# Kernel optimization log

Hardware: AMD Instinct MI355X
Metric: run time of the kernel (lower is better)

## Reference

```python
import jax, jax.numpy as jnp
import numpy as np

D_MODEL, N_HEADS, D_FF, THETA, EPS = 1024, 16, 4096, 10000.0, 1e-5
D_K = D_MODEL // N_HEADS


def setup_inputs() -> dict:
    key = jax.random.key(0)
    ks = jax.random.split(key, 10)

    def lin(k, out_f, in_f):
        sigma = np.sqrt(2.0 / (in_f + out_f))
        return (jax.random.truncated_normal(k, -3.0, 3.0, (out_f, in_f), jnp.float32) * sigma)

    return {
        'in_features': jax.random.normal(ks[0], (2, 2048, D_MODEL), jnp.float32),
        'Wq': lin(ks[1], D_MODEL, D_MODEL),
        'Wk': lin(ks[2], D_MODEL, D_MODEL),
        'Wv': lin(ks[3], D_MODEL, D_MODEL),
        'Wo': lin(ks[4], D_MODEL, D_MODEL),
        'ln1_w': jnp.ones((D_MODEL,), jnp.float32),
        'ln2_w': jnp.ones((D_MODEL,), jnp.float32),
        'w1': lin(ks[5], D_FF, D_MODEL),
        'w2': lin(ks[6], D_MODEL, D_FF),
        'w3': lin(ks[7], D_FF, D_MODEL),
    }


def _rmsnorm(x, w):
    xf = x.astype(jnp.float32)
    out = xf * jax.lax.rsqrt(jnp.mean(xf * xf, axis=-1, keepdims=True) + EPS) * w
    return out.astype(x.dtype)


def _rope(x, positions):
    # x: [b, h, s, d_k]; rotate pairs (2k, 2k+1) by angle pos / theta^(2k/d_k)
    k = jnp.arange(D_K // 2, dtype=jnp.float32)
    inv_freq = jnp.power(THETA, -2.0 * k / D_K)              # [d_k/2]
    ang = positions[:, None].astype(jnp.float32) * inv_freq  # [s, d_k/2]
    cos, sin = jnp.cos(ang), jnp.sin(ang)
    x_e, x_o = x[..., 0::2], x[..., 1::2]
    out_e = x_e * cos - x_o * sin
    out_o = x_e * sin + x_o * cos
    return jnp.stack([out_e, out_o], axis=-1).reshape(x.shape)


def _attention(x, Wq, Wk, Wv, Wo):
    b, s, _ = x.shape
    pos = jnp.arange(s)

    def heads(W):
        h = jnp.einsum('bsd,ed->bse', x, W)
        return h.reshape(b, s, N_HEADS, D_K).transpose(0, 2, 1, 3)  # [b,h,s,dk]

    q = _rope(heads(Wq), pos)
    k = _rope(heads(Wk), pos)
    v = heads(Wv)
    scores = jnp.einsum('bhqd,bhkd->bhqk', q, k) / jnp.sqrt(jnp.float32(D_K))
    causal = jnp.tril(jnp.ones((s, s), bool))
    scores = jnp.where(causal, scores, -jnp.inf)
    probs = jax.nn.softmax(scores, axis=-1)
    ctx = jnp.einsum('bhqk,bhkd->bhqd', probs, v)
    ctx = ctx.transpose(0, 2, 1, 3).reshape(b, s, D_MODEL)
    return jnp.einsum('bsv,dv->bsd', ctx, Wo)


def _swiglu(x, w1, w2, w3):
    a = jnp.einsum('bsd,fd->bsf', x, w1)
    g = jnp.einsum('bsd,fd->bsf', x, w3)
    return jnp.einsum('bsf,df->bsd', (a * jax.nn.sigmoid(a)) * g, w2)


def reference(in_features, Wq, Wk, Wv, Wo, ln1_w, ln2_w, w1, w2, w3):
    x = in_features + _attention(_rmsnorm(in_features, ln1_w), Wq, Wk, Wv, Wo)
    return x + _swiglu(_rmsnorm(x, ln2_w), w1, w2, w3)
```

## Files before the change

kernel.cpp:

```cpp
#include <hip/hip_runtime.h>
#include <hip/hip_bf16.h>
#include <math.h>


#define S_SEQ 2048
#define DM    1024
#define NH    16
#define DK    64
#define DFF   4096
#define T_TOK 4096

typedef short s16x8 __attribute__((ext_vector_type(8)));
typedef float f32x4 __attribute__((ext_vector_type(4)));

__device__ __forceinline__ unsigned short f32_to_bf16_rn(float f) {
  unsigned int u = __float_as_uint(f);
  unsigned int r = (u + 0x7FFFu + ((u >> 16) & 1u)) >> 16;
  return (unsigned short)r;
}
__device__ __forceinline__ float bf16_to_f32(unsigned short h) {
  return __uint_as_float(((unsigned int)h) << 16);
}

__device__ __forceinline__ void gload_lds16(const void* g, void* l) {
  __builtin_amdgcn_global_load_lds(
      (const __attribute__((address_space(1))) void*)g,
      (__attribute__((address_space(3))) void*)l, 16, 0, 0);
}

__global__ __launch_bounds__(256) void rmsnorm_planes(
    const float* __restrict__ x, const float* __restrict__ w,
    unsigned short* __restrict__ oh, unsigned short* __restrict__ ol)
{
  const int row = blockIdx.x;
  const int tid = threadIdx.x;
  const float4 v = ((const float4*)(x + (size_t)row * DM))[tid];
  float ss = v.x * v.x + v.y * v.y + v.z * v.z + v.w * v.w;
#pragma unroll
  for (int off = 32; off > 0; off >>= 1) ss += __shfl_xor(ss, off);
  __shared__ float red[4];
  if ((tid & 63) == 0) red[tid >> 6] = ss;
  __syncthreads();
  const float total = red[0] + red[1] + red[2] + red[3];
  const float scale = rsqrtf(total * (1.0f / DM) + 1e-5f);
  const float4 wv = ((const float4*)w)[tid];
  const float o0 = v.x * scale * wv.x, o1 = v.y * scale * wv.y;
  const float o2 = v.z * scale * wv.z, o3 = v.w * scale * wv.w;
  ushort4 h, l;
  h.x = f32_to_bf16_rn(o0); l.x = f32_to_bf16_rn(o0 - bf16_to_f32(h.x));
  h.y = f32_to_bf16_rn(o1); l.y = f32_to_bf16_rn(o1 - bf16_to_f32(h.y));
  h.z = f32_to_bf16_rn(o2); l.z = f32_to_bf16_rn(o2 - bf16_to_f32(h.z));
  h.w = f32_to_bf16_rn(o3); l.w = f32_to_bf16_rn(o3 - bf16_to_f32(h.w));
  ((ushort4*)(oh + (size_t)row * DM))[tid] = h;
  ((ushort4*)(ol + (size_t)row * DM))[tid] = l;
}

__global__ __launch_bounds__(256) void split_planes(
    const float* __restrict__ x, unsigned short* __restrict__ oh,
    unsigned short* __restrict__ ol, int n4)
{
  const int i = blockIdx.x * 256 + threadIdx.x;
  if (i >= n4) return;
  const float4 v = ((const float4*)x)[i];
  ushort4 h, l;
  h.x = f32_to_bf16_rn(v.x); l.x = f32_to_bf16_rn(v.x - bf16_to_f32(h.x));
  h.y = f32_to_bf16_rn(v.y); l.y = f32_to_bf16_rn(v.y - bf16_to_f32(h.y));
  h.z = f32_to_bf16_rn(v.z); l.z = f32_to_bf16_rn(v.z - bf16_to_f32(h.z));
  h.w = f32_to_bf16_rn(v.w); l.w = f32_to_bf16_rn(v.w - bf16_to_f32(h.w));
  ((ushort4*)oh)[i] = h;
  ((ushort4*)ol)[i] = l;
}

template <int MODE>
__global__ __launch_bounds__(256, 2) void gemm_sb(
    const unsigned short* __restrict__ Ah, const unsigned short* __restrict__ Al,
    const unsigned short* __restrict__ Bh, const unsigned short* __restrict__ Bl,
    const float* __restrict__ auxF,
    const unsigned short* __restrict__ auxH, const unsigned short* __restrict__ auxL,
    float* __restrict__ Cf, unsigned short* __restrict__ CH, unsigned short* __restrict__ CL,
    int N, int Kiter, int LDA, int LDB)
{
  __shared__ __align__(128) char lds[32768];
  constexpr int AHo = 0, ALo = 8192, BHo = 16384, BLo = 24576;

  const int nbn = N >> 7;
  int bid = blockIdx.x;
  const int cpx = gridDim.x >> 3;
  bid = (bid & 7) * cpx + (bid >> 3);
  const int bmi = bid / nbn;
  const int bm = bmi << 7;
  const int bn = (bid - bmi * nbn) << 7;

  const int tid  = threadIdx.x;
  const int lane = tid & 63;
  const int wave = tid >> 6;
  const int wr = (wave >> 1) << 6;
  const int wc = (wave & 1) << 6;
  const int lrow = lane & 15;
  const int lk   = lane >> 4;

  const int idx0 = tid, idx1 = tid + 256;
  const int r0 = idx0 >> 2, r1 = idx1 >> 2;
  const int c0 = idx0 & 3,  c1 = idx1 & 3;
  const size_t a0 = (size_t)(bm + r0) * LDA + c0 * 8;
  const size_t a1 = (size_t)(bm + r1) * LDA + c1 * 8;
  const size_t b0 = (size_t)(bn + r0) * LDB + c0 * 8;
  const size_t b1 = (size_t)(bn + r1) * LDB + c1 * 8;
  char* d0 = lds + idx0 * 16;
  char* d1 = lds + idx1 * 16;

  const int fro = lrow * 64 + (lk << 4);
  const char* pA = lds + AHo + wr * 64 + fro;
  const char* pB = lds + BHo + wc * 64 + fro;

  f32x4 acc[4][4] = {};

  for (int k0 = 0; k0 < Kiter; k0 += 32) {
    gload_lds16(Ah + a0 + k0, d0 + AHo);
    gload_lds16(Ah + a1 + k0, d1 + AHo);
    gload_lds16(Al + a0 + k0, d0 + ALo);
    gload_lds16(Al + a1 + k0, d1 + ALo);
    gload_lds16(Bh + b0 + k0, d0 + BHo);
    gload_lds16(Bh + b1 + k0, d1 + BHo);
    gload_lds16(Bl + b0 + k0, d0 + BLo);
    gload_lds16(Bl + b1 + k0, d1 + BLo);
    __syncthreads();

    s16x8 aH[4], aL[4], bH[4], bL[4];
#pragma unroll
    for (int f = 0; f < 4; ++f) {
      aH[f] = *(const s16x8*)(pA + f * 1024);
      aL[f] = *(const s16x8*)(pA + f * 1024 + (ALo - AHo));
      bH[f] = *(const s16x8*)(pB + f * 1024);
      bL[f] = *(const s16x8*)(pB + f * 1024 + (BLo - BHo));
    }
#pragma unroll
    for (int mi = 0; mi < 4; ++mi)
#pragma unroll
      for (int ni = 0; ni < 4; ++ni) {
        acc[mi][ni] = __builtin_amdgcn_mfma_f32_16x16x32_bf16(aH[mi], bH[ni], acc[mi][ni], 0, 0, 0);
        acc[mi][ni] = __builtin_amdgcn_mfma_f32_16x16x32_bf16(aH[mi], bL[ni], acc[mi][ni], 0, 0, 0);
        acc[mi][ni] = __builtin_amdgcn_mfma_f32_16x16x32_bf16(aL[mi], bH[ni], acc[mi][ni], 0, 0, 0);
      }
    __syncthreads();
  }

#pragma unroll
  for (int mi = 0; mi < 4; ++mi) {
#pragma unroll
    for (int r = 0; r < 4; ++r) {
      const int row = bm + wr + mi * 16 + lk * 4 + r;
      const size_t rowo = (size_t)row * N;
#pragma unroll
      for (int ni = 0; ni < 4; ++ni) {
        const int col = bn + wc + ni * 16 + lrow;
        float v = acc[mi][ni][r];
        if constexpr (MODE == 1) v += auxF[rowo + col];
        if constexpr (MODE == 2) v = v / (1.0f + expf(-v));
        if constexpr (MODE == 3)
          v *= bf16_to_f32(auxH[rowo + col]) + bf16_to_f32(auxL[rowo + col]);
        if constexpr (MODE >= 2) {
          const unsigned short hb = f32_to_bf16_rn(v);
          CH[rowo + col] = hb;
          CL[rowo + col] = f32_to_bf16_rn(v - bf16_to_f32(hb));
        } else {
          Cf[rowo + col] = v;
        }
      }
    }
  }
}

__global__ __launch_bounds__(256) void rope_table(float* __restrict__ tab)
{
  const int idx = blockIdx.x * 256 + threadIdx.x;
  const int pos = idx >> 5;
  const int i = idx & 31;
  const float ivf = (float)pow(10000.0, -(double)i / 32.0);
  const float angf = (float)((double)pos * (double)ivf);
  double sn, cs;
  sincos((double)angf, &sn, &cs);
  tab[idx * 2]     = (float)cs;
  tab[idx * 2 + 1] = (float)sn;
}

__global__ __launch_bounds__(256) void rope_apply_planes(
    unsigned short* __restrict__ QH, unsigned short* __restrict__ QL,
    unsigned short* __restrict__ KH, unsigned short* __restrict__ KL,
    const float* __restrict__ tab)
{
  const int t = blockIdx.x;
  const int pos = t & (S_SEQ - 1);
  const size_t rb = (size_t)t * DM;
#pragma unroll
  for (int it = 0; it < 2; ++it) {
    const int p = threadIdx.x + it * 256;
    const int i = p & 31;
    const int off = ((p >> 5) << 6) + (i << 1);
    const float2 cst = ((const float2*)tab)[pos * 32 + i];
    const float c = cst.x, s = cst.y;
#pragma unroll
    for (int qk = 0; qk < 2; ++qk) {
      unsigned short* H = qk ? KH : QH;
      unsigned short* L = qk ? KL : QL;
      const unsigned int vh = *(unsigned int*)(H + rb + off);
      const unsigned int vl = *(unsigned int*)(L + rb + off);
      const float e = bf16_to_f32((unsigned short)(vh & 0xffff)) +
                      bf16_to_f32((unsigned short)(vl & 0xffff));
      const float o = bf16_to_f32((unsigned short)(vh >> 16)) +
                      bf16_to_f32((unsigned short)(vl >> 16));
      const float ne = e * c - o * s;
      const float no = e * s + o * c;
      const unsigned short h0 = f32_to_bf16_rn(ne), h1 = f32_to_bf16_rn(no);
      const unsigned short l0 = f32_to_bf16_rn(ne - bf16_to_f32(h0));
      const unsigned short l1 = f32_to_bf16_rn(no - bf16_to_f32(h1));
      *(unsigned int*)(H + rb + off) = (unsigned)h0 | ((unsigned)h1 << 16);
      *(unsigned int*)(L + rb + off) = (unsigned)l0 | ((unsigned)l1 << 16);
    }
  }
}

__global__ __launch_bounds__(256) void vt_split(
    const float* __restrict__ Vf, unsigned short* __restrict__ VtH,
    unsigned short* __restrict__ VtL)
{
  __shared__ float T[64][65];
  const int b = blockIdx.z, h = blockIdx.y, s0 = blockIdx.x * 64;
  const int tid = threadIdx.x;
#pragma unroll
  for (int p = 0; p < 4; ++p) {
    const int idx = p * 256 + tid;
    const int s = idx >> 4;
    const int d4 = (idx & 15) << 2;
    const float4 v = *(const float4*)(Vf + (size_t)(b * S_SEQ + s0 + s) * DM + h * 64 + d4);
    T[s][d4] = v.x; T[s][d4 + 1] = v.y; T[s][d4 + 2] = v.z; T[s][d4 + 3] = v.w;
  }
  __syncthreads();
  const int d = tid >> 2;
  const int sc = (tid & 3) << 4;
  unsigned int hw[8], lw[8];
#pragma unroll
  for (int j = 0; j < 8; ++j) {
    const float v0 = T[sc + 2 * j][d], v1 = T[sc + 2 * j + 1][d];
    const unsigned short h0 = f32_to_bf16_rn(v0), h1 = f32_to_bf16_rn(v1);
    const unsigned short l0 = f32_to_bf16_rn(v0 - bf16_to_f32(h0));
    const unsigned short l1 = f32_to_bf16_rn(v1 - bf16_to_f32(h1));
    hw[j] = (unsigned)h0 | ((unsigned)h1 << 16);
    lw[j] = (unsigned)l0 | ((unsigned)l1 << 16);
  }
  const size_t base = ((size_t)((b * NH + h) * 64 + d)) * S_SEQ + s0 + sc;
#pragma unroll
  for (int j = 0; j < 8; ++j) {
    *(unsigned int*)(VtH + base + 2 * j) = hw[j];
    *(unsigned int*)(VtL + base + 2 * j) = lw[j];
  }
}

__global__ __launch_bounds__(256, 3) void attn_mfma(
    const unsigned short* __restrict__ QH, const unsigned short* __restrict__ QL,
    const unsigned short* __restrict__ KH, const unsigned short* __restrict__ KL,
    const unsigned short* __restrict__ VtH, const unsigned short* __restrict__ VtL,
    unsigned short* __restrict__ ctxH, unsigned short* __restrict__ ctxL)
{
  __shared__ __align__(128) char lds[51200];
  const int h = blockIdx.y, b = blockIdx.z;
  const int qt = 31 - blockIdx.x;
  const int q0 = qt << 6;
  const int tid = threadIdx.x;
  const int lane = tid & 63;
  const int w = tid >> 6;
  const int lg = lane >> 4;
  const int lr = lane & 15;

  const size_t qtok = (size_t)(b * S_SEQ + q0 + w * 16 + lr);
  s16x8 qh[2], ql[2];
#pragma unroll
  for (int kc = 0; kc < 2; ++kc) {
    const size_t off = qtok * DM + h * 64 + kc * 32 + lg * 8;
    qh[kc] = *(const s16x8*)(QH + off);
    ql[kc] = *(const s16x8*)(QL + off);
  }

  f32x4 acc[4] = {};
  float mrow[4], lsum[4];
#pragma unroll
  for (int r = 0; r < 4; ++r) { mrow[r] = -1e30f; lsum[r] = 0.f; }

  unsigned short* PH = (unsigned short*)(lds + 32768 + w * 4608);
  unsigned short* PL = PH + 1152;
  const int wmax = q0 + w * 16 + 15;
  const int ntiles = qt + 1;

  for (int t = 0; t < ntiles; ++t) {
    const int kt = t << 6;
#pragma unroll
    for (int pp = 0; pp < 8; ++pp) {
      const int idx = pp * 256 + tid;
      const int plane = idx >> 9;
      const int ci = idx & 511;
      const int row = ci >> 3, pc = ci & 7;
      const int lc = pc ^ (row & 7);
      const unsigned short* src;
      if (plane == 0)      src = KH + (size_t)(b * S_SEQ + kt + row) * DM + h * 64 + lc * 8;
      else if (plane == 1) src = KL + (size_t)(b * S_SEQ + kt + row) * DM + h * 64 + lc * 8;
      else if (plane == 2) src = VtH + ((size_t)((b * NH + h) * 64 + row)) * S_SEQ + kt + lc * 8;
      else                 src = VtL + ((size_t)((b * NH + h) * 64 + row)) * S_SEQ + kt + lc * 8;
      gload_lds16(src, lds + plane * 8192 + ci * 16);
    }
    __syncthreads();

    if (kt <= wmax) {
      f32x4 s[4] = {};
      __builtin_amdgcn_s_setprio(1);
#pragma unroll
      for (int nf = 0; nf < 4; ++nf) {
        const int key = nf * 16 + lr;
#pragma unroll
        for (int kc = 0; kc < 2; ++kc) {
          const int pcx = (kc * 4 + lg) ^ (key & 7);
          const char* base = lds + key * 128 + pcx * 16;
          const s16x8 kh = *(const s16x8*)(base);
          const s16x8 kl = *(const s16x8*)(base + 8192);
          s[nf] = __builtin_amdgcn_mfma_f32_16x16x32_bf16(qh[kc], kh, s[nf], 0, 0, 0);
          s[nf] = __builtin_amdgcn_mfma_f32_16x16x32_bf16(qh[kc], kl, s[nf], 0, 0, 0);
          s[nf] = __builtin_amdgcn_mfma_f32_16x16x32_bf16(ql[kc], kh, s[nf], 0, 0, 0);
        }
      }
      __builtin_amdgcn_s_setprio(0);
      const int myrow = q0 + w * 16 + 4 * lg;
#pragma unroll
      for (int nf = 0; nf < 4; ++nf) {
        const int key = kt + nf * 16 + lr;
#pragma unroll
        for (int r = 0; r < 4; ++r) {
          const float sv = s[nf][r] * 0.125f;
          s[nf][r] = (key <= myrow + r) ? sv : -__builtin_inff();
        }
      }
#pragma unroll
      for (int r = 0; r < 4; ++r) {
        float mx = fmaxf(fmaxf(s[0][r], s[1][r]), fmaxf(s[2][r], s[3][r]));
        mx = fmaxf(mx, __shfl_xor(mx, 1));
        mx = fmaxf(mx, __shfl_xor(mx, 2));
        mx = fmaxf(mx, __shfl_xor(mx, 4));
        mx = fmaxf(mx, __shfl_xor(mx, 8));
        const float mn = fmaxf(mrow[r], mx);
        const float corr = __expf(mrow[r] - mn);
        mrow[r] = mn;
        float ps = 0.f;
#pragma unroll
        for (int nf = 0; nf < 4; ++nf) {
          const float pv = __expf(s[nf][r] - mn);
          s[nf][r] = pv;
          ps += pv;
        }
        ps += __shfl_xor(ps, 1); ps += __shfl_xor(ps, 2);
        ps += __shfl_xor(ps, 4); ps += __shfl_xor(ps, 8);
        lsum[r] = lsum[r] * corr + ps;
#pragma unroll
        for (int nf = 0; nf < 4; ++nf) acc[nf][r] *= corr;
      }
#pragma unroll
      for (int nf = 0; nf < 4; ++nf)
#pragma unroll
        for (int r = 0; r < 4; ++r) {
          const float pv = s[nf][r];
          const unsigned short ph = f32_to_bf16_rn(pv);
          const unsigned short pl = f32_to_bf16_rn(pv - bf16_to_f32(ph));
          const int pidx = (4 * lg + r) * 72 + nf * 16 + lr;
          PH[pidx] = ph; PL[pidx] = pl;
        }
      __builtin_amdgcn_s_setprio(1);
#pragma unroll
      for (int kc = 0; kc < 2; ++kc) {
        const int eoff = lr * 72 + kc * 32 + lg * 8;
        const s16x8 pa = *(const s16x8*)(PH + eoff);
        const s16x8 pb = *(const s16x8*)(PL + eoff);
#pragma unroll
        for (int nf = 0; nf < 4; ++nf) {
          const int d = nf * 16 + lr;
          const int pcx = (kc * 4 + lg) ^ (d & 7);
          const char* vb = lds + 16384 + d * 128 + pcx * 16;
          const s16x8 vh = *(const s16x8*)(vb);
          const s16x8 vl = *(const s16x8*)(vb + 8192);
          acc[nf] = __builtin_amdgcn_mfma_f32_16x16x32_bf16(pa, vh, acc[nf], 0, 0, 0);
          acc[nf] = __builtin_amdgcn_mfma_f32_16x16x32_bf16(pa, vl, acc[nf], 0, 0, 0);
          acc[nf] = __builtin_amdgcn_mfma_f32_16x16x32_bf16(pb, vh, acc[nf], 0, 0, 0);
        }
      }
      __builtin_amdgcn_s_setprio(0);
    }
    __syncthreads();
  }
#pragma unroll
  for (int r = 0; r < 4; ++r) {
    const float inv = 1.0f / lsum[r];
    const size_t tok = (size_t)(b * S_SEQ + q0 + w * 16 + 4 * lg + r);
#pragma unroll
    for (int nf = 0; nf < 4; ++nf) {
      const float v = acc[nf][r] * inv;
      const unsigned short hb = f32_to_bf16_rn(v);
      const size_t o = tok * DM + h * 64 + nf * 16 + lr;
      ctxH[o] = hb;
      ctxL[o] = f32_to_bf16_rn(v - bf16_to_f32(hb));
    }
  }
}

extern "C" void kernel_launch(void* const* d_in, const int* in_sizes, int n_in,
                              void* d_out, int out_size, void* d_ws, size_t ws_size,
                              hipStream_t stream)
{
  const float* x   = (const float*)d_in[0];
  const float* Wq  = (const float*)d_in[1];
  const float* Wk  = (const float*)d_in[2];
  const float* Wv  = (const float*)d_in[3];
  const float* Wo  = (const float*)d_in[4];
  const float* ln1 = (const float*)d_in[5];
  const float* ln2 = (const float*)d_in[6];
  const float* w1  = (const float*)d_in[7];
  const float* w2  = (const float*)d_in[8];
  const float* w3  = (const float*)d_in[9];
  float* out = (float*)d_out;
  char* ws = (char*)d_ws;
  const size_t MB = 1024 * 1024;

  unsigned short* WqH = (unsigned short*)(ws + 0 * MB);
  unsigned short* WqL = (unsigned short*)(ws + 2 * MB);
  unsigned short* WkH = (unsigned short*)(ws + 4 * MB);
  unsigned short* WkL = (unsigned short*)(ws + 6 * MB);
  unsigned short* WvH = (unsigned short*)(ws + 8 * MB);
  unsigned short* WvL = (unsigned short*)(ws + 10 * MB);
  unsigned short* WoH = (unsigned short*)(ws + 12 * MB);
  unsigned short* WoL = (unsigned short*)(ws + 14 * MB);
  unsigned short* w1H = (unsigned short*)(ws + 16 * MB);
  unsigned short* w1L = (unsigned short*)(ws + 24 * MB);
  unsigned short* w2H = (unsigned short*)(ws + 32 * MB);
  unsigned short* w2L = (unsigned short*)(ws + 40 * MB);
  unsigned short* w3H = (unsigned short*)(ws + 48 * MB);
  unsigned short* w3L = (unsigned short*)(ws + 56 * MB);
  unsigned short* hH  = (unsigned short*)(ws + 64 * MB);
  unsigned short* hL  = (unsigned short*)(ws + 72 * MB);
  unsigned short* QHp = (unsigned short*)(ws + 80 * MB);
  unsigned short* QLp = (unsigned short*)(ws + 88 * MB);
  unsigned short* KHp = (unsigned short*)(ws + 96 * MB);
  unsigned short* KLp = (unsigned short*)(ws + 104 * MB);
  float* Vf = (float*)(ws + 112 * MB);
  float* tab = (float*)(ws + 128 * MB);
  unsigned short* VtH = (unsigned short*)(ws + 128 * MB);
  unsigned short* VtL = (unsigned short*)(ws + 136 * MB);
  unsigned short* ctxH = (unsigned short*)(ws + 144 * MB);
  unsigned short* ctxL = (unsigned short*)(ws + 152 * MB);
  float* x2 = (float*)(ws + 80 * MB);
  unsigned short* t1H = (unsigned short*)(ws + 96 * MB);
  unsigned short* t1L = (unsigned short*)(ws + 112 * MB);
  unsigned short* uH  = (unsigned short*)(ws + 128 * MB);
  unsigned short* uL  = (unsigned short*)(ws + 144 * MB);

  rope_table<<<256, 256, 0, stream>>>(tab);
  split_planes<<<1024, 256, 0, stream>>>(Wq, WqH, WqL, 1024 * 1024 / 4);
  split_planes<<<1024, 256, 0, stream>>>(Wk, WkH, WkL, 1024 * 1024 / 4);
  split_planes<<<1024, 256, 0, stream>>>(Wv, WvH, WvL, 1024 * 1024 / 4);
  split_planes<<<1024, 256, 0, stream>>>(Wo, WoH, WoL, 1024 * 1024 / 4);
  split_planes<<<4096, 256, 0, stream>>>(w1, w1H, w1L, 4096 * 1024 / 4);
  split_planes<<<4096, 256, 0, stream>>>(w2, w2H, w2L, 4096 * 1024 / 4);
  split_planes<<<4096, 256, 0, stream>>>(w3, w3H, w3L, 4096 * 1024 / 4);

  rmsnorm_planes<<<T_TOK, 256, 0, stream>>>(x, ln1, hH, hL);
  gemm_sb<4><<<256, 256, 0, stream>>>(hH, hL, WqH, WqL, nullptr, nullptr, nullptr, nullptr, QHp, QLp, DM, DM, DM, DM);
  gemm_sb<4><<<256, 256, 0, stream>>>(hH, hL, WkH, WkL, nullptr, nullptr, nullptr, nullptr, KHp, KLp, DM, DM, DM, DM);
  gemm_sb<0><<<256, 256, 0, stream>>>(hH, hL, WvH, WvL, nullptr, nullptr, nullptr, Vf, nullptr, nullptr, DM, DM, DM, DM);
  rope_apply_planes<<<T_TOK, 256, 0, stream>>>(QHp, QLp, KHp, KLp, tab);
  vt_split<<<dim3(32, NH, 2), 256, 0, stream>>>(Vf, VtH, VtL);
  attn_mfma<<<dim3(32, NH, 2), 256, 0, stream>>>(QHp, QLp, KHp, KLp, VtH, VtL, ctxH, ctxL);
  gemm_sb<1><<<256, 256, 0, stream>>>(ctxH, ctxL, WoH, WoL, x, nullptr, nullptr, x2, nullptr, nullptr, DM, DM, DM, DM);
  rmsnorm_planes<<<T_TOK, 256, 0, stream>>>(x2, ln2, hH, hL);
  for (int f = 0; f < 2; ++f) {
    const unsigned short* w1Hf = w1H + (size_t)f * 2048 * 1024;
    const unsigned short* w1Lf = w1L + (size_t)f * 2048 * 1024;
    const unsigned short* w3Hf = w3H + (size_t)f * 2048 * 1024;
    const unsigned short* w3Lf = w3L + (size_t)f * 2048 * 1024;
    gemm_sb<2><<<512, 256, 0, stream>>>(hH, hL, w1Hf, w1Lf, nullptr, nullptr, nullptr, nullptr, t1H, t1L, 2048, DM, DM, DM);
    gemm_sb<3><<<512, 256, 0, stream>>>(hH, hL, w3Hf, w3Lf, nullptr, t1H, t1L, nullptr, uH, uL, 2048, DM, DM, DM);
    gemm_sb<1><<<256, 256, 0, stream>>>(uH, uL, w2H + (size_t)f * 2048, w2L + (size_t)f * 2048,
                                        (f == 0 ? x2 : out), nullptr, nullptr, out, nullptr, nullptr,
                                        DM, 2048, 2048, DFF);
  }
}
```

Before: 932.5 us.

## Replace GEMMs with double-buffered 256-row 8-wave kernel, fuse QKV, pair attention tiles

Replaces the 128x128 GEMM with a 512-thread kernel using 256xBN tiles, a double-buffered LDS prefetch pipeline with swizzled layout, and explicit waitcnt/barrier scheduling. Q, K and V projections are fused into one GEMM writing bf16 planes (V no longer fp32). The FFN is no longer chunked in two halves, and the gate product is done in place. Attention blocks now each process a short and a long causal query tile to balance work. Fewer, larger blocks may underfill the 256 CUs for the 1024-wide outputs.

```diff
diff --git a/kernel.cpp b/kernel.cpp
--- a/kernel.cpp
+++ b/kernel.cpp
@@ -6,7 +6,6 @@
 #define S_SEQ 2048
 #define DM    1024
 #define NH    16
-#define DK    64
 #define DFF   4096
 #define T_TOK 4096
 
@@ -71,100 +70,162 @@
   ((ushort4*)ol)[i] = l;
 }
 
-template <int MODE>
-__global__ __launch_bounds__(256, 2) void gemm_sb(
+template <int BN, int MODE>
+__global__ __launch_bounds__(512, 2) void gemm8(
     const unsigned short* __restrict__ Ah, const unsigned short* __restrict__ Al,
     const unsigned short* __restrict__ Bh, const unsigned short* __restrict__ Bl,
-    const float* __restrict__ auxF,
-    const unsigned short* __restrict__ auxH, const unsigned short* __restrict__ auxL,
-    float* __restrict__ Cf, unsigned short* __restrict__ CH, unsigned short* __restrict__ CL,
-    int N, int Kiter, int LDA, int LDB)
-{
-  __shared__ __align__(128) char lds[32768];
-  constexpr int AHo = 0, ALo = 8192, BHo = 16384, BLo = 24576;
-
-  const int nbn = N >> 7;
+    const float* __restrict__ auxF, float* __restrict__ Cf,
+    unsigned short* __restrict__ CH, unsigned short* __restrict__ CL,
+    unsigned short* __restrict__ C2H, unsigned short* __restrict__ C2L,
+    unsigned short* __restrict__ C3H, unsigned short* __restrict__ C3L,
+    int N, int K, int LDA, int LDB, int nbn)
+{
+  constexpr int NF = BN / 64;
+  constexpr int WNS = BN / 4;
+  constexpr int ABYT = 256 * 32 * 2;
+  constexpr int BBYT = BN * 32 * 2;
+  constexpr int AHo = 0, ALo = ABYT, BHo = 2 * ABYT, BLo = 2 * ABYT + BBYT;
+  constexpr int BUFSZ = 2 * ABYT + 2 * BBYT;
+  __shared__ __align__(128) char lds[2 * BUFSZ];
+
+  const int tid = threadIdx.x;
+  const int lane = tid & 63;
+  const int wave = tid >> 6;
+  const int wm = wave >> 2, wn = wave & 3;
+  const int lr = lane & 15, lg = lane >> 4;
+  const int koff = ((lg ^ ((lr >> 1) & 3)) << 4);
+
   int bid = blockIdx.x;
   const int cpx = gridDim.x >> 3;
   bid = (bid & 7) * cpx + (bid >> 3);
   const int bmi = bid / nbn;
-  const int bm = bmi << 7;
-  const int bn = (bid - bmi * nbn) << 7;
-
-  const int tid  = threadIdx.x;
-  const int lane = tid & 63;
-  const int wave = tid >> 6;
-  const int wr = (wave >> 1) << 6;
-  const int wc = (wave & 1) << 6;
-  const int lrow = lane & 15;
-  const int lk   = lane >> 4;
-
-  const int idx0 = tid, idx1 = tid + 256;
-  const int r0 = idx0 >> 2, r1 = idx1 >> 2;
-  const int c0 = idx0 & 3,  c1 = idx1 & 3;
-  const size_t a0 = (size_t)(bm + r0) * LDA + c0 * 8;
-  const size_t a1 = (size_t)(bm + r1) * LDA + c1 * 8;
-  const size_t b0 = (size_t)(bn + r0) * LDB + c0 * 8;
-  const size_t b1 = (size_t)(bn + r1) * LDB + c1 * 8;
-  char* d0 = lds + idx0 * 16;
-  char* d1 = lds + idx1 * 16;
-
-  const int fro = lrow * 64 + (lk << 4);
-  const char* pA = lds + AHo + wr * 64 + fro;
-  const char* pB = lds + BHo + wc * 64 + fro;
-
-  f32x4 acc[4][4] = {};
-
-  for (int k0 = 0; k0 < Kiter; k0 += 32) {
-    gload_lds16(Ah + a0 + k0, d0 + AHo);
-    gload_lds16(Ah + a1 + k0, d1 + AHo);
-    gload_lds16(Al + a0 + k0, d0 + ALo);
-    gload_lds16(Al + a1 + k0, d1 + ALo);
-    gload_lds16(Bh + b0 + k0, d0 + BHo);
-    gload_lds16(Bh + b1 + k0, d1 + BHo);
-    gload_lds16(Bl + b0 + k0, d0 + BLo);
-    gload_lds16(Bl + b1 + k0, d1 + BLo);
-    __syncthreads();
-
-    s16x8 aH[4], aL[4], bH[4], bL[4];
-#pragma unroll
-    for (int f = 0; f < 4; ++f) {
-      aH[f] = *(const s16x8*)(pA + f * 1024);
-      aL[f] = *(const s16x8*)(pA + f * 1024 + (ALo - AHo));
-      bH[f] = *(const s16x8*)(pB + f * 1024);
-      bL[f] = *(const s16x8*)(pB + f * 1024 + (BLo - BHo));
+  const int bm = bmi << 8;
+  const int bn = (bid - bmi * nbn) * BN;
+
+  const int cA0 = tid, cA1 = tid + 512;
+  const int rA0 = cA0 >> 2, rA1 = cA1 >> 2;
+  const int sA0 = (bm + rA0) * LDA + (((cA0 & 3) ^ ((rA0 >> 1) & 3)) << 3);
+  const int sA1 = (bm + rA1) * LDA + (((cA1 & 3) ^ ((rA1 >> 1) & 3)) << 3);
+  const int dA0 = cA0 * 16, dA1 = cA1 * 16;
+  const int rB0 = cA0 >> 2;
+  const int sB0 = (bn + rB0) * LDB + (((cA0 & 3) ^ ((rB0 >> 1) & 3)) << 3);
+  const int dB0 = cA0 * 16;
+  const int rB1 = cA1 >> 2;
+  const int sB1 = (bn + rB1) * LDB + (((cA1 & 3) ^ ((rB1 >> 1) & 3)) << 3);
+  const int dB1 = cA1 * 16;
+
+  f32x4 acc[8][NF] = {};
+
+  gload_lds16(Ah + sA0, lds + AHo + dA0);
+  gload_lds16(Ah + sA1, lds + AHo + dA1);
+  gload_lds16(Al + sA0, lds + ALo + dA0);
+  gload_lds16(Al + sA1, lds + ALo + dA1);
+  gload_lds16(Bh + sB0, lds + BHo + dB0);
+  if constexpr (BN == 256) gload_lds16(Bh + sB1, lds + BHo + dB1);
+  gload_lds16(Bl + sB0, lds + BLo + dB0);
+  if constexpr (BN == 256) gload_lds16(Bl + sB1, lds + BLo + dB1);
+
+  const int NT = K >> 5;
+  const int arow = (wm * 128 + lr) * 64 + koff;
+  const int brow = (wn * WNS + lr) * 64 + koff;
+
+  for (int t = 0; t < NT; ++t) {
+    char* L  = lds + (t & 1) * BUFSZ;
+    char* Ln = lds + ((t + 1) & 1) * BUFSZ;
+    const int kn = (t + 1) << 5;
+    const bool pf = (t + 1 < NT);
+    s16x8 bh[NF], bl[NF];
+
+#pragma unroll
+    for (int p = 0; p < 4; ++p) {
+      if (p == 0 && pf) {
+        gload_lds16(Ah + sA0 + kn, Ln + AHo + dA0);
+        gload_lds16(Ah + sA1 + kn, Ln + AHo + dA1);
+      }
+      if (p == 1 && pf) {
+        gload_lds16(Al + sA0 + kn, Ln + ALo + dA0);
+        gload_lds16(Al + sA1 + kn, Ln + ALo + dA1);
+      }
+      if (p == 2 && pf) {
+        gload_lds16(Bh + sB0 + kn, Ln + BHo + dB0);
+        if constexpr (BN == 256) gload_lds16(Bh + sB1 + kn, Ln + BHo + dB1);
+      }
+      if (p == 3 && pf) {
+        gload_lds16(Bl + sB0 + kn, Ln + BLo + dB0);
+        if constexpr (BN == 256) gload_lds16(Bl + sB1 + kn, Ln + BLo + dB1);
+      }
+      if (p == 0) {
+        if (pf) asm volatile("s_waitcnt vmcnt(2)" ::: "memory");
+        else    asm volatile("s_waitcnt vmcnt(0)" ::: "memory");
+        __builtin_amdgcn_sched_barrier(0);
+        __builtin_amdgcn_s_barrier();
+      }
+      if (p == 0) {
+#pragma unroll
+        for (int nf = 0; nf < NF; ++nf) {
+          bh[nf] = *(const s16x8*)(L + BHo + brow + nf * 1024);
+          bl[nf] = *(const s16x8*)(L + BLo + brow + nf * 1024);
+        }
+      }
+      const s16x8 a0h = *(const s16x8*)(L + AHo + arow + p * 2048);
+      const s16x8 a0l = *(const s16x8*)(L + ALo + arow + p * 2048);
+      const s16x8 a1h = *(const s16x8*)(L + AHo + arow + p * 2048 + 1024);
+      const s16x8 a1l = *(const s16x8*)(L + ALo + arow + p * 2048 + 1024);
+      asm volatile("s_waitcnt lgkmcnt(0)" ::: "memory");
+      __builtin_amdgcn_sched_barrier(0);
+      __builtin_amdgcn_s_setprio(1);
+#pragma unroll
+      for (int nf = 0; nf < NF; ++nf) {
+        acc[2 * p][nf] = __builtin_amdgcn_mfma_f32_16x16x32_bf16(a0h, bh[nf], acc[2 * p][nf], 0, 0, 0);
+        acc[2 * p][nf] = __builtin_amdgcn_mfma_f32_16x16x32_bf16(a0h, bl[nf], acc[2 * p][nf], 0, 0, 0);
+        acc[2 * p][nf] = __builtin_amdgcn_mfma_f32_16x16x32_bf16(a0l, bh[nf], acc[2 * p][nf], 0, 0, 0);
+        acc[2 * p + 1][nf] = __builtin_amdgcn_mfma_f32_16x16x32_bf16(a1h, bh[nf], acc[2 * p + 1][nf], 0, 0, 0);
+        acc[2 * p + 1][nf] = __builtin_amdgcn_mfma_f32_16x16x32_bf16(a1h, bl[nf], acc[2 * p + 1][nf], 0, 0, 0);
+        acc[2 * p + 1][nf] = __builtin_amdgcn_mfma_f32_16x16x32_bf16(a1l, bh[nf], acc[2 * p + 1][nf], 0, 0, 0);
+      }
+      __builtin_amdgcn_s_setprio(0);
+      __builtin_amdgcn_s_barrier();
     }
-#pragma unroll
-    for (int mi = 0; mi < 4; ++mi)
-#pragma unroll
-      for (int ni = 0; ni < 4; ++ni) {
-        acc[mi][ni] = __builtin_amdgcn_mfma_f32_16x16x32_bf16(aH[mi], bH[ni], acc[mi][ni], 0, 0, 0);
-        acc[mi][ni] = __builtin_amdgcn_mfma_f32_16x16x32_bf16(aH[mi], bL[ni], acc[mi][ni], 0, 0, 0);
-        acc[mi][ni] = __builtin_amdgcn_mfma_f32_16x16x32_bf16(aL[mi], bH[ni], acc[mi][ni], 0, 0, 0);
-      }
-    __syncthreads();
-  }
-
-#pragma unroll
-  for (int mi = 0; mi < 4; ++mi) {
+  }
+
+  unsigned short* oH = CH;
+  unsigned short* oL = CL;
+  int coff = 0;
+  if constexpr (MODE == 5) {
+    const int seg = bn >> 10;
+    coff = seg << 10;
+    if (seg == 1) { oH = C2H; oL = C2L; }
+    else if (seg == 2) { oH = C3H; oL = C3L; }
+  }
+#pragma unroll
+  for (int mf = 0; mf < 8; ++mf) {
 #pragma unroll
     for (int r = 0; r < 4; ++r) {
-      const int row = bm + wr + mi * 16 + lk * 4 + r;
-      const size_t rowo = (size_t)row * N;
-#pragma unroll
-      for (int ni = 0; ni < 4; ++ni) {
-        const int col = bn + wc + ni * 16 + lrow;
-        float v = acc[mi][ni][r];
-        if constexpr (MODE == 1) v += auxF[rowo + col];
-        if constexpr (MODE == 2) v = v / (1.0f + expf(-v));
-        if constexpr (MODE == 3)
-          v *= bf16_to_f32(auxH[rowo + col]) + bf16_to_f32(auxL[rowo + col]);
-        if constexpr (MODE >= 2) {
+      const int row = bm + wm * 128 + mf * 16 + lg * 4 + r;
+#pragma unroll
+      for (int nf = 0; nf < NF; ++nf) {
+        const int col = bn + wn * WNS + nf * 16 + lr;
+        float v = acc[mf][nf][r];
+        if constexpr (MODE == 1) {
+          const size_t idx = (size_t)row * N + col;
+          Cf[idx] = auxF[idx] + v;
+        } else if constexpr (MODE == 2) {
+          const size_t idx = (size_t)row * N + col;
+          v = v / (1.0f + expf(-v));
           const unsigned short hb = f32_to_bf16_rn(v);
-          CH[rowo + col] = hb;
-          CL[rowo + col] = f32_to_bf16_rn(v - bf16_to_f32(hb));
+          CH[idx] = hb;
+          CL[idx] = f32_to_bf16_rn(v - bf16_to_f32(hb));
+        } else if constexpr (MODE == 3) {
+          const size_t idx = (size_t)row * N + col;
+          v *= bf16_to_f32(CH[idx]) + bf16_to_f32(CL[idx]);
+          const unsigned short hb = f32_to_bf16_rn(v);
+          CH[idx] = hb;
+          CL[idx] = f32_to_bf16_rn(v - bf16_to_f32(hb));
         } else {
-          Cf[rowo + col] = v;
+          const size_t idx = (size_t)row * 1024 + (col - coff);
+          const unsigned short hb = f32_to_bf16_rn(v);
+          oH[idx] = hb;
+          oL[idx] = f32_to_bf16_rn(v - bf16_to_f32(hb));
         }
       }
     }
@@ -221,8 +282,8 @@
 }
 
 __global__ __launch_bounds__(256) void vt_split(
-    const float* __restrict__ Vf, unsigned short* __restrict__ VtH,
-    unsigned short* __restrict__ VtL)
+    const unsigned short* __restrict__ VH, const unsigned short* __restrict__ VL,
+    unsigned short* __restrict__ VtH, unsigned short* __restrict__ VtL)
 {
   __shared__ float T[64][65];
   const int b = blockIdx.z, h = blockIdx.y, s0 = blockIdx.x * 64;
@@ -232,8 +293,13 @@
     const int idx = p * 256 + tid;
     const int s = idx >> 4;
     const int d4 = (idx & 15) << 2;
-    const float4 v = *(const float4*)(Vf + (size_t)(b * S_SEQ + s0 + s) * DM + h * 64 + d4);
-    T[s][d4] = v.x; T[s][d4 + 1] = v.y; T[s][d4 + 2] = v.z; T[s][d4 + 3] = v.w;
+    const size_t g = (size_t)(b * S_SEQ + s0 + s) * DM + h * 64 + d4;
+    const ushort4 a = *(const ushort4*)(VH + g);
+    const ushort4 c = *(const ushort4*)(VL + g);
+    T[s][d4]     = bf16_to_f32(a.x) + bf16_to_f32(c.x);
+    T[s][d4 + 1] = bf16_to_f32(a.y) + bf16_to_f32(c.y);
+    T[s][d4 + 2] = bf16_to_f32(a.z) + bf16_to_f32(c.z);
+    T[s][d4 + 3] = bf16_to_f32(a.w) + bf16_to_f32(c.w);
   }
   __syncthreads();
   const int d = tid >> 2;
@@ -264,145 +330,149 @@
 {
   __shared__ __align__(128) char lds[51200];
   const int h = blockIdx.y, b = blockIdx.z;
-  const int qt = 31 - blockIdx.x;
-  const int q0 = qt << 6;
   const int tid = threadIdx.x;
   const int lane = tid & 63;
   const int w = tid >> 6;
   const int lg = lane >> 4;
   const int lr = lane & 15;
 
-  const size_t qtok = (size_t)(b * S_SEQ + q0 + w * 16 + lr);
-  s16x8 qh[2], ql[2];
-#pragma unroll
-  for (int kc = 0; kc < 2; ++kc) {
-    const size_t off = qtok * DM + h * 64 + kc * 32 + lg * 8;
-    qh[kc] = *(const s16x8*)(QH + off);
-    ql[kc] = *(const s16x8*)(QL + off);
-  }
-
-  f32x4 acc[4] = {};
-  float mrow[4], lsum[4];
-#pragma unroll
-  for (int r = 0; r < 4; ++r) { mrow[r] = -1e30f; lsum[r] = 0.f; }
-
   unsigned short* PH = (unsigned short*)(lds + 32768 + w * 4608);
   unsigned short* PL = PH + 1152;
-  const int wmax = q0 + w * 16 + 15;
-  const int ntiles = qt + 1;
-
-  for (int t = 0; t < ntiles; ++t) {
-    const int kt = t << 6;
-#pragma unroll
-    for (int pp = 0; pp < 8; ++pp) {
-      const int idx = pp * 256 + tid;
-      const int plane = idx >> 9;
-      const int ci = idx & 511;
-      const int row = ci >> 3, pc = ci & 7;
-      const int lc = pc ^ (row & 7);
-      const unsigned short* src;
-      if (plane == 0)      src = KH + (size_t)(b * S_SEQ + kt + row) * DM + h * 64 + lc * 8;
-      else if (plane == 1) src = KL + (size_t)(b * S_SEQ + kt + row) * DM + h * 64 + lc * 8;
-      else if (plane == 2) src = VtH + ((size_t)((b * NH + h) * 64 + row)) * S_SEQ + kt + lc * 8;
-      else                 src = VtL + ((size_t)((b * NH + h) * 64 + row)) * S_SEQ + kt + lc * 8;
-      gload_lds16(src, lds + plane * 8192 + ci * 16);
+
+  for (int pi = 0; pi < 2; ++pi) {
+    const int qt = pi ? (31 - blockIdx.x) : blockIdx.x;
+    const int q0 = qt << 6;
+
+    const size_t qtok = (size_t)(b * S_SEQ + q0 + w * 16 + lr);
+    s16x8 qh[2], ql[2];
+#pragma unroll
+    for (int kc = 0; kc < 2; ++kc) {
+      const size_t off = qtok * DM + h * 64 + kc * 32 + lg * 8;
+      qh[kc] = *(const s16x8*)(QH + off);
+      ql[kc] = *(const s16x8*)(QL + off);
     }
-    __syncthreads();
-
-    if (kt <= wmax) {
-      f32x4 s[4] = {};
-      __builtin_amdgcn_s_setprio(1);
+
+    f32x4 acc[4] = {};
+    float mrow[4], lsum[4];
+#pragma unroll
+    for (int r = 0; r < 4; ++r) { mrow[r] = -1e30f; lsum[r] = 0.f; }
+
+    const int wmax = q0 + w * 16 + 15;
+    const int ntiles = qt + 1;
+
+    for (int t = 0; t < ntiles; ++t) {
+      const int kt = t << 6;
+#pragma unroll
+      for (int pp = 0; pp < 8; ++pp) {
+        const int idx = pp * 256 + tid;
+        const int plane = idx >> 9;
+        const int ci = idx & 511;
+        const int row = ci >> 3, pc = ci & 7;
+        const int lc = pc ^ (row & 7);
+        const unsigned short* src;
+        if (plane == 0)      src = KH + (size_t)(b * S_SEQ + kt + row) * DM + h * 64 + lc * 8;
+        else if (plane == 1) src = KL + (size_t)(b * S_SEQ + kt + row) * DM + h * 64 + lc * 8;
+        else if (plane == 2) src = VtH + ((size_t)((b * NH + h) * 64 + row)) * S_SEQ + kt + lc * 8;
+        else                 src = VtL + ((size_t)((b * NH + h) * 64 + row)) * S_SEQ + kt + lc * 8;
+        gload_lds16(src, lds + plane * 8192 + ci * 16);
+      }
+      __syncthreads();
+
+      if (kt <= wmax) {
+        f32x4 s[4] = {};
+        __builtin_amdgcn_s_setprio(1);
+#pragma unroll
+        for (int nf = 0; nf < 4; ++nf) {
+          const int key = nf * 16 + lr;
+#pragma unroll
+          for (int kc = 0; kc < 2; ++kc) {
+            const int pcx = (kc * 4 + lg) ^ (key & 7);
+            const char* base = lds + key * 128 + pcx * 16;
+            const s16x8 kh = *(const s16x8*)(base);
+            const s16x8 kl = *(const s16x8*)(base + 8192);
+            s[nf] = __builtin_amdgcn_mfma_f32_16x16x32_bf16(qh[kc], kh, s[nf], 0, 0, 0);
+            s[nf] = __builtin_amdgcn_mfma_f32_16x16x32_bf16(qh[kc], kl, s[nf], 0, 0, 0);
+            s[nf] = __builtin_amdgcn_mfma_f32_16x16x32_bf16(ql[kc], kh, s[nf], 0, 0, 0);
+          }
+        }
+        __builtin_amdgcn_s_setprio(0);
+        const int myrow = q0 + w * 16 + 4 * lg;
+#pragma unroll
+        for (int nf = 0; nf < 4; ++nf) {
+          const int key = kt + nf * 16 + lr;
+#pragma unroll
+          for (int r = 0; r < 4; ++r) {
+            const float sv = s[nf][r] * 0.125f;
+            s[nf][r] = (key <= myrow + r) ? sv : -__builtin_inff();
+          }
+        }
+#pragma unroll
+        for (int r = 0; r < 4; ++r) {
+          float mx = fmaxf(fmaxf(s[0][r], s[1][r]), fmaxf(s[2][r], s[3][r]));
+          mx = fmaxf(mx, __shfl_xor(mx, 1));
+          mx = fmaxf(mx, __shfl_xor(mx, 2));
+          mx = fmaxf(mx, __shfl_xor(mx, 4));
+          mx = fmaxf(mx, __shfl_xor(mx, 8));
+          const float mn = fmaxf(mrow[r], mx);
+          const float corr = __expf(mrow[r] - mn);
+          mrow[r] = mn;
+          float ps = 0.f;
+#pragma unroll
+          for (int nf = 0; nf < 4; ++nf) {
+            const float pv = __expf(s[nf][r] - mn);
+            s[nf][r] = pv;
+            ps += pv;
+          }
+          ps += __shfl_xor(ps, 1); ps += __shfl_xor(ps, 2);
+          ps += __shfl_xor(ps, 4); ps += __shfl_xor(ps, 8);
+          lsum[r] = lsum[r] * corr + ps;
+#pragma unroll
+          for (int nf = 0; nf < 4; ++nf) acc[nf][r] *= corr;
+        }
+#pragma unroll
+        for (int nf = 0; nf < 4; ++nf)
+#pragma unroll
+          for (int r = 0; r < 4; ++r) {
+            const float pv = s[nf][r];
+            const unsigned short ph = f32_to_bf16_rn(pv);
+            const unsigned short pl = f32_to_bf16_rn(pv - bf16_to_f32(ph));
+            const int pidx = (4 * lg + r) * 72 + nf * 16 + lr;
+            PH[pidx] = ph; PL[pidx] = pl;
+          }
+        __builtin_amdgcn_s_setprio(1);
+#pragma unroll
+        for (int kc = 0; kc < 2; ++kc) {
+          const int eoff = lr * 72 + kc * 32 + lg * 8;
+          const s16x8 pa = *(const s16x8*)(PH + eoff);
+          const s16x8 pb = *(const s16x8*)(PL + eoff);
+#pragma unroll
+          for (int nf = 0; nf < 4; ++nf) {
+            const int d = nf * 16 + lr;
+            const int pcx = (kc * 4 + lg) ^ (d & 7);
+            const char* vb = lds + 16384 + d * 128 + pcx * 16;
+            const s16x8 vh = *(const s16x8*)(vb);
+            const s16x8 vl = *(const s16x8*)(vb + 8192);
+            acc[nf] = __builtin_amdgcn_mfma_f32_16x16x32_bf16(pa, vh, acc[nf], 0, 0, 0);
+            acc[nf] = __builtin_amdgcn_mfma_f32_16x16x32_bf16(pa, vl, acc[nf], 0, 0, 0);
+            acc[nf] = __builtin_amdgcn_mfma_f32_16x16x32_bf16(pb, vh, acc[nf], 0, 0, 0);
+          }
+        }
+        __builtin_amdgcn_s_setprio(0);
+      }
+      __syncthreads();
+    }
+#pragma unroll
+    for (int r = 0; r < 4; ++r) {
+      const float inv = 1.0f / lsum[r];
+      const size_t tok = (size_t)(b * S_SEQ + q0 + w * 16 + 4 * lg + r);
 #pragma unroll
       for (int nf = 0; nf < 4; ++nf) {
-        const int key = nf * 16 + lr;
-#pragma unroll
-        for (int kc = 0; kc < 2; ++kc) {
-          const int pcx = (kc * 4 + lg) ^ (key & 7);
-          const char* base = lds + key * 128 + pcx * 16;
-          const s16x8 kh = *(const s16x8*)(base);
-          const s16x8 kl = *(const s16x8*)(base + 8192);
-          s[nf] = __builtin_amdgcn_mfma_f32_16x16x32_bf16(qh[kc], kh, s[nf], 0, 0, 0);
-          s[nf] = __builtin_amdgcn_mfma_f32_16x16x32_bf16(qh[kc], kl, s[nf], 0, 0, 0);
-          s[nf] = __builtin_amdgcn_mfma_f32_16x16x32_bf16(ql[kc], kh, s[nf], 0, 0, 0);
-        }
-      }
-      __builtin_amdgcn_s_setprio(0);
-      const int myrow = q0 + w * 16 + 4 * lg;
-#pragma unroll
-      for (int nf = 0; nf < 4; ++nf) {
-        const int key = kt + nf * 16 + lr;
-#pragma unroll
-        for (int r = 0; r < 4; ++r) {
-          const float sv = s[nf][r] * 0.125f;
-          s[nf][r] = (key <= myrow + r) ? sv : -__builtin_inff();
-        }
-      }
-#pragma unroll
-      for (int r = 0; r < 4; ++r) {
-        float mx = fmaxf(fmaxf(s[0][r], s[1][r]), fmaxf(s[2][r], s[3][r]));
-        mx = fmaxf(mx, __shfl_xor(mx, 1));
-        mx = fmaxf(mx, __shfl_xor(mx, 2));
-        mx = fmaxf(mx, __shfl_xor(mx, 4));
-        mx = fmaxf(mx, __shfl_xor(mx, 8));
-        const float mn = fmaxf(mrow[r], mx);
-        const float corr = __expf(mrow[r] - mn);
-        mrow[r] = mn;
-        float ps = 0.f;
-#pragma unroll
-        for (int nf = 0; nf < 4; ++nf) {
-          const float pv = __expf(s[nf][r] - mn);
-          s[nf][r] = pv;
-          ps += pv;
-        }
-        ps += __shfl_xor(ps, 1); ps += __shfl_xor(ps, 2);
-        ps += __shfl_xor(ps, 4); ps += __shfl_xor(ps, 8);
-        lsum[r] = lsum[r] * corr + ps;
-#pragma unroll
-        for (int nf = 0; nf < 4; ++nf) acc[nf][r] *= corr;
-      }
-#pragma unroll
-      for (int nf = 0; nf < 4; ++nf)
-#pragma unroll
-        for (int r = 0; r < 4; ++r) {
-          const float pv = s[nf][r];
-          const unsigned short ph = f32_to_bf16_rn(pv);
-          const unsigned short pl = f32_to_bf16_rn(pv - bf16_to_f32(ph));
-          const int pidx = (4 * lg + r) * 72 + nf * 16 + lr;
-          PH[pidx] = ph; PL[pidx] = pl;
-        }
-      __builtin_amdgcn_s_setprio(1);
-#pragma unroll
-      for (int kc = 0; kc < 2; ++kc) {
-        const int eoff = lr * 72 + kc * 32 + lg * 8;
-        const s16x8 pa = *(const s16x8*)(PH + eoff);
-        const s16x8 pb = *(const s16x8*)(PL + eoff);
-#pragma unroll
-        for (int nf = 0; nf < 4; ++nf) {
-          const int d = nf * 16 + lr;
-          const int pcx = (kc * 4 + lg) ^ (d & 7);
-          const char* vb = lds + 16384 + d * 128 + pcx * 16;
-          const s16x8 vh = *(const s16x8*)(vb);
-          const s16x8 vl = *(const s16x8*)(vb + 8192);
-          acc[nf] = __builtin_amdgcn_mfma_f32_16x16x32_bf16(pa, vh, acc[nf], 0, 0, 0);
-          acc[nf] = __builtin_amdgcn_mfma_f32_16x16x32_bf16(pa, vl, acc[nf], 0, 0, 0);
-          acc[nf] = __builtin_amdgcn_mfma_f32_16x16x32_bf16(pb, vh, acc[nf], 0, 0, 0);
-        }
-      }
-      __builtin_amdgcn_s_setprio(0);
-    }
-    __syncthreads();
-  }
-#pragma unroll
-  for (int r = 0; r < 4; ++r) {
-    const float inv = 1.0f / lsum[r];
-    const size_t tok = (size_t)(b * S_SEQ + q0 + w * 16 + 4 * lg + r);
-#pragma unroll
-    for (int nf = 0; nf < 4; ++nf) {
-      const float v = acc[nf][r] * inv;
-      const unsigned short hb = f32_to_bf16_rn(v);
-      const size_t o = tok * DM + h * 64 + nf * 16 + lr;
-      ctxH[o] = hb;
-      ctxL[o] = f32_to_bf16_rn(v - bf16_to_f32(hb));
+        const float v = acc[nf][r] * inv;
+        const unsigned short hb = f32_to_bf16_rn(v);
+        const size_t o = tok * DM + h * 64 + nf * 16 + lr;
+        ctxH[o] = hb;
+        ctxL[o] = f32_to_bf16_rn(v - bf16_to_f32(hb));
+      }
     }
   }
 }
@@ -425,12 +495,8 @@
   char* ws = (char*)d_ws;
   const size_t MB = 1024 * 1024;
 
-  unsigned short* WqH = (unsigned short*)(ws + 0 * MB);
-  unsigned short* WqL = (unsigned short*)(ws + 2 * MB);
-  unsigned short* WkH = (unsigned short*)(ws + 4 * MB);
-  unsigned short* WkL = (unsigned short*)(ws + 6 * MB);
-  unsigned short* WvH = (unsigned short*)(ws + 8 * MB);
-  unsigned short* WvL = (unsigned short*)(ws + 10 * MB);
+  unsigned short* WqkvH = (unsigned short*)(ws + 0 * MB);
+  unsigned short* WqkvL = (unsigned short*)(ws + 6 * MB);
   unsigned short* WoH = (unsigned short*)(ws + 12 * MB);
   unsigned short* WoL = (unsigned short*)(ws + 14 * MB);
   unsigned short* w1H = (unsigned short*)(ws + 16 * MB);
@@ -445,45 +511,44 @@
   unsigned short* QLp = (unsigned short*)(ws + 88 * MB);
   unsigned short* KHp = (unsigned short*)(ws + 96 * MB);
   unsigned short* KLp = (unsigned short*)(ws + 104 * MB);
-  float* Vf = (float*)(ws + 112 * MB);
-  float* tab = (float*)(ws + 128 * MB);
+  unsigned short* VHp = (unsigned short*)(ws + 112 * MB);
+  unsigned short* VLp = (unsigned short*)(ws + 120 * MB);
   unsigned short* VtH = (unsigned short*)(ws + 128 * MB);
   unsigned short* VtL = (unsigned short*)(ws + 136 * MB);
   unsigned short* ctxH = (unsigned short*)(ws + 144 * MB);
   unsigned short* ctxL = (unsigned short*)(ws + 152 * MB);
-  float* x2 = (float*)(ws + 80 * MB);
-  unsigned short* t1H = (unsigned short*)(ws + 96 * MB);
-  unsigned short* t1L = (unsigned short*)(ws + 112 * MB);
-  unsigned short* uH  = (unsigned short*)(ws + 128 * MB);
-  unsigned short* uL  = (unsigned short*)(ws + 144 * MB);
+  float* tab = (float*)(ws + 159 * MB + 512 * 1024);
+  float* x2  = (float*)(ws + 112 * MB);
+  unsigned short* t1H = (unsigned short*)(ws + 80 * MB);
+  unsigned short* t1L = (unsigned short*)(ws + 128 * MB);
 
   rope_table<<<256, 256, 0, stream>>>(tab);
-  split_planes<<<1024, 256, 0, stream>>>(Wq, WqH, WqL, 1024 * 1024 / 4);
-  split_planes<<<1024, 256, 0, stream>>>(Wk, WkH, WkL, 1024 * 1024 / 4);
-  split_planes<<<1024, 256, 0, stream>>>(Wv, WvH, WvL, 1024 * 1024 / 4);
+  split_planes<<<1024, 256, 0, stream>>>(Wq, WqkvH, WqkvL, 1024 * 1024 / 4);
+  split_planes<<<1024, 256, 0, stream>>>(Wk, WqkvH + 1024 * 1024, WqkvL + 1024 * 1024, 1024 * 1024 / 4);
+  split_planes<<<1024, 256, 0, stream>>>(Wv, WqkvH + 2048 * 1024, WqkvL + 2048 * 1024, 1024 * 1024 / 4);
   split_planes<<<1024, 256, 0, stream>>>(Wo, WoH, WoL, 1024 * 1024 / 4);
   split_planes<<<4096, 256, 0, stream>>>(w1, w1H, w1L, 4096 * 1024 / 4);
   split_planes<<<4096, 256, 0, stream>>>(w2, w2H, w2L, 4096 * 1024 / 4);
   split_planes<<<4096, 256, 0, stream>>>(w3, w3H, w3L, 4096 * 1024 / 4);
 
   rmsnorm_planes<<<T_TOK, 256, 0, stream>>>(x, ln1, hH, hL);
-  gemm_sb<4><<<256, 256, 0, stream>>>(hH, hL, WqH, WqL, nullptr, nullptr, nullptr, nullptr, QHp, QLp, DM, DM, DM, DM);
-  gemm_sb<4><<<256, 256, 0, stream>>>(hH, hL, WkH, WkL, nullptr, nullptr, nullptr, nullptr, KHp, KLp, DM, DM, DM, DM);
-  gemm_sb<0><<<256, 256, 0, stream>>>(hH, hL, WvH, WvL, nullptr, nullptr, nullptr, Vf, nullptr, nullptr, DM, DM, DM, DM);
+  gemm8<256, 5><<<192, 512, 0, stream>>>(hH, hL, WqkvH, WqkvL, nullptr, nullptr,
+                                         QHp, QLp, KHp, KLp, VHp, VLp,
+                                         3072, DM, DM, DM, 12);
   rope_apply_planes<<<T_TOK, 256, 0, stream>>>(QHp, QLp, KHp, KLp, tab);
-  vt_split<<<dim3(32, NH, 2), 256, 0, stream>>>(Vf, VtH, VtL);
-  attn_mfma<<<dim3(32, NH, 2), 256, 0, stream>>>(QHp, QLp, KHp, KLp, VtH, VtL, ctxH, ctxL);
-  gemm_sb<1><<<256, 256, 0, stream>>>(ctxH, ctxL, WoH, WoL, x, nullptr, nullptr, x2, nullptr, nullptr, DM, DM, DM, DM);
+  vt_split<<<dim3(32, NH, 2), 256, 0, stream>>>(VHp, VLp, VtH, VtL);
+  attn_mfma<<<dim3(16, NH, 2), 256, 0, stream>>>(QHp, QLp, KHp, KLp, VtH, VtL, ctxH, ctxL);
+  gemm8<128, 1><<<128, 512, 0, stream>>>(ctxH, ctxL, WoH, WoL, x, x2,
+                                         nullptr, nullptr, nullptr, nullptr, nullptr, nullptr,
+                                         DM, DM, DM, DM, 8);
   rmsnorm_planes<<<T_TOK, 256, 0, stream>>>(x2, ln2, hH, hL);
-  for (int f = 0; f < 2; ++f) {
-    const unsigned short* w1Hf = w1H + (size_t)f * 2048 * 1024;
-    const unsigned short* w1Lf = w1L + (size_t)f * 2048 * 1024;
-    const unsigned short* w3Hf = w3H + (size_t)f * 2048 * 1024;
-    const unsigned short* w3Lf = w3L + (size_t)f * 2048 * 1024;
-    gemm_sb<2><<<512, 256, 0, stream>>>(hH, hL, w1Hf, w1Lf, nullptr, nullptr, nullptr, nullptr, t1H, t1L, 2048, DM, DM, DM);
-    gemm_sb<3><<<512, 256, 0, stream>>>(hH, hL, w3Hf, w3Lf, nullptr, t1H, t1L, nullptr, uH, uL, 2048, DM, DM, DM);
-    gemm_sb<1><<<256, 256, 0, stream>>>(uH, uL, w2H + (size_t)f * 2048, w2L + (size_t)f * 2048,
-                                        (f == 0 ? x2 : out), nullptr, nullptr, out, nullptr, nullptr,
-                                        DM, 2048, 2048, DFF);
-  }
-}
+  gemm8<256, 2><<<256, 512, 0, stream>>>(hH, hL, w1H, w1L, nullptr, nullptr,
+                                         t1H, t1L, nullptr, nullptr, nullptr, nullptr,
+                                         DFF, DM, DM, DM, 16);
+  gemm8<256, 3><<<256, 512, 0, stream>>>(hH, hL, w3H, w3L, nullptr, nullptr,
+                                         t1H, t1L, nullptr, nullptr, nullptr, nullptr,
+                                         DFF, DM, DM, DM, 16);
+  gemm8<128, 1><<<128, 512, 0, stream>>>(t1H, t1L, w2H, w2L, x2, out,
+                                         nullptr, nullptr, nullptr, nullptr, nullptr, nullptr,
+                                         DM, DFF, DFF, DFF, 8);
+}
```

Measured after the change: 749.4 us. 1.24x faster.
